# Kernel optimization log

Measured on AMD Instinct MI355X. Metric: run time of the kernel, lower is better.

## Reference

```python
import jax, jax.numpy as jnp
import numpy as np

N_NODES = 100000
N_EDGES = 1600000
IN_FEATS = 128
HIDDEN = 128


def _graph_conv(x, W, b, src, dst, n_nodes):
    # DGL GraphConv with norm='both': out = D_in^{-1/2} * A^T * (D_out^{-1/2} * x) @ W + b
    ones = jnp.ones((src.shape[0],), dtype=x.dtype)
    deg_out = jax.ops.segment_sum(ones, src, num_segments=n_nodes)
    deg_in = jax.ops.segment_sum(ones, dst, num_segments=n_nodes)
    norm_src = jax.lax.rsqrt(jnp.clip(deg_out, 1.0))  # [N]
    norm_dst = jax.lax.rsqrt(jnp.clip(deg_in, 1.0))   # [N]
    h = x @ W                                          # [N, F_out]
    msg = h[src] * norm_src[src][:, None]              # gather by edge src: [E, F_out]
    agg = jax.ops.segment_sum(msg, dst, num_segments=n_nodes)  # scatter-add to dst
    return agg * norm_dst[:, None] + b


def setup_inputs() -> dict:
    key = jax.random.key(0)
    ks = jax.random.split(key, 9)
    x = jax.random.normal(ks[0], (N_NODES, IN_FEATS), dtype=jnp.float32)
    src = jax.random.randint(ks[1], (N_EDGES,), 0, N_NODES, dtype=jnp.int32)
    dst = jax.random.randint(ks[2], (N_EDGES,), 0, N_NODES, dtype=jnp.int32)
    s1 = 1.0 / np.sqrt(IN_FEATS)
    s2 = 1.0 / np.sqrt(HIDDEN)
    W1 = jax.random.uniform(ks[3], (IN_FEATS, HIDDEN), jnp.float32, -s1, s1)
    b1 = jnp.zeros((HIDDEN,), jnp.float32)
    W2 = jax.random.uniform(ks[4], (HIDDEN, HIDDEN), jnp.float32, -s2, s2)
    b2 = jnp.zeros((HIDDEN,), jnp.float32)
    sp = 1.0 / np.sqrt(2 * HIDDEN)
    Wp = jax.random.uniform(ks[5], (2 * HIDDEN, 1), jnp.float32, -sp, sp)
    bp = jax.random.uniform(ks[6], (1,), jnp.float32, -sp, sp)
    return {"x": x, "W1": W1, "b1": b1, "W2": W2, "b2": b2,
            "Wp": Wp, "bp": bp, "src": src, "dst": dst}


def reference(x, W1, b1, W2, b2, Wp, bp, src, dst):
    n_nodes = x.shape[0]
    h = _graph_conv(x, W1, b1, src, dst, n_nodes)
    h = jax.nn.relu(h)
    h = _graph_conv(h, W2, b2, src, dst, n_nodes)  # final node embeddings [N, H]
    # predict_links on the same edge list: cat(h[u], h[v]) -> linear -> sigmoid
    edge_h = jnp.concatenate([h[src], h[dst]], axis=1)  # [E, 2H]
    scores = jax.nn.sigmoid(edge_h @ Wp + bp)           # [E, 1]
    return scores
```

## Files before the change

kernel.cpp:

```cpp
#include <hip/hip_runtime.h>
#include <cstdint>
#include <cstddef>

#define NN 100000
#define NE 1600000
#define F  128
#define NPAD 100352
#define NBUCK 3125
#define BCAPG 768
#define CHUNK 4167

typedef __attribute__((ext_vector_type(8))) short bf16x8;
typedef __attribute__((ext_vector_type(4))) float f32x4;

__device__ __forceinline__ unsigned short f2bf(float f) {
    unsigned u = __float_as_uint(f);
    unsigned r = (u + 0x7fffu + ((u >> 16) & 1u)) >> 16;
    return (unsigned short)r;
}
__device__ __forceinline__ void acc_bf8s(const uint4 v, const float ns, float* acc) {
    acc[0] += __uint_as_float(v.x << 16) * ns;
    acc[1] += __uint_as_float(v.x & 0xffff0000u) * ns;
    acc[2] += __uint_as_float(v.y << 16) * ns;
    acc[3] += __uint_as_float(v.y & 0xffff0000u) * ns;
    acc[4] += __uint_as_float(v.z << 16) * ns;
    acc[5] += __uint_as_float(v.z & 0xffff0000u) * ns;
    acc[6] += __uint_as_float(v.w << 16) * ns;
    acc[7] += __uint_as_float(v.w & 0xffff0000u) * ns;
}

__global__ void setup_kernel(int* __restrict__ gCur,
                             const float* __restrict__ W2, const float* __restrict__ Wp,
                             const float* __restrict__ b2, const float* __restrict__ bp,
                             float* __restrict__ consts, float2* __restrict__ V) {
    const int g = blockIdx.x;
    const int tid = threadIdx.x;
    if (g < 13) {
        const int b = g * 256 + tid;
        if (b < NBUCK) gCur[b] = b * BCAPG;
        return;
    }
    if (tid < 128) {
        float sa = 0.f, sc = 0.f;
        #pragma unroll 8
        for (int j = 0; j < F; ++j) {
            const float w = W2[tid * F + j];
            sa += w * Wp[j];
            sc += w * Wp[F + j];
        }
        V[tid] = make_float2(sa, sc);
    } else if (tid < 192) {
        const int l = tid - 128;
        const float2 bb = *(const float2*)&b2[2 * l];
        const float2 wa = *(const float2*)&Wp[2 * l];
        const float2 wc = *(const float2*)&Wp[F + 2 * l];
        float s = bb.x * (wa.x + wc.x) + bb.y * (wa.y + wc.y);
        #pragma unroll
        for (int m = 32; m > 0; m >>= 1) s += __shfl_xor(s, m);
        if (l == 0) consts[0] = s + bp[0];
    }
}

__global__ __launch_bounds__(256, 3)
void gemm1_fill_kernel(const float* __restrict__ in, const float* __restrict__ W,
                       unsigned short* __restrict__ out_bf,
                       const int* __restrict__ src, const int* __restrict__ dst,
                       int* __restrict__ deg_out, int* __restrict__ gCur,
                       int* __restrict__ srcPart) {
    __shared__ __align__(16) char smem[50016];

    const int g = blockIdx.x;
    const int tid = threadIdx.x;

    if (g & 1) {
        int* packedL = (int*)smem;
        unsigned short* bktL = (unsigned short*)(packedL + CHUNK);
        int* hist = (int*)(smem + 25008);
        int* curL = hist + NBUCK;
        const int e0 = (g >> 1) * CHUNK;
        const int nCh = min(CHUNK, NE - e0);
        for (int i = tid; i < NBUCK; i += 256) hist[i] = 0;
        __syncthreads();
        for (int i = tid; i < nCh; i += 256) {
            const int s = src[e0 + i];
            const int d = dst[e0 + i];
            atomicAdd(&deg_out[s], 1);
            const int bkt = d >> 5;
            atomicAdd(&hist[bkt], 1);
            packedL[i] = s | ((d & 31) << 17);
            bktL[i] = (unsigned short)bkt;
        }
        __syncthreads();
        for (int b = tid; b < NBUCK; b += 256) {
            const int c = hist[b];
            curL[b] = (c > 0) ? atomicAdd(&gCur[b], c) : 0;
        }
        __syncthreads();
        for (int i = tid; i < nCh; i += 256) {
            const int bkt = bktL[i];
            const int p = atomicAdd(&curL[bkt], 1);
            if (p < (bkt + 1) * BCAPG)
                srcPart[p] = packedL[i];
        }
        return;
    }

    char* A_s = smem;

    const int gid  = g >> 1;
    const int w    = tid >> 6;
    const int lane = tid & 63;
    const int ml   = lane & 15;
    const int quad = lane >> 4;

    bf16x8 Bf[4][2];
    #pragma unroll
    for (int kb = 0; kb < 4; ++kb) {
        #pragma unroll
        for (int nb = 0; nb < 2; ++nb) {
            const int n = 32 * w + nb * 16 + ml;
            const int k0 = kb * 32 + quad * 8;
            #pragma unroll
            for (int j = 0; j < 8; ++j)
                Bf[kb][nb][j] = (short)f2bf(W[(k0 + j) * F + n]);
        }
    }

    const int nTiles = NN / 32;
    for (int tile = gid; tile < nTiles; tile += 384) {
        const int row0 = tile * 32;
        __syncthreads();
        #pragma unroll
        for (int c = 0; c < 2; ++c) {
            const int i2 = tid + 256 * c;
            const int m  = i2 >> 4;
            const int o  = i2 & 15;
            const float* xr = &in[(size_t)(row0 + m) * F + o * 8];
            const float4 v0 = *(const float4*)xr;
            const float4 v1 = *(const float4*)(xr + 4);
            short h8[8];
            h8[0] = (short)f2bf(v0.x); h8[1] = (short)f2bf(v0.y);
            h8[2] = (short)f2bf(v0.z); h8[3] = (short)f2bf(v0.w);
            h8[4] = (short)f2bf(v1.x); h8[5] = (short)f2bf(v1.y);
            h8[6] = (short)f2bf(v1.z); h8[7] = (short)f2bf(v1.w);
            const int kb2 = o >> 2, q2 = o & 3, ml2 = m & 15, mh2 = m >> 4;
            const int fo = (((mh2 * 4 + kb2) * 64) + q2 * 16 + ml2) * 16;
            *(bf16x8*)(A_s + fo) = *(bf16x8*)h8;
        }
        __syncthreads();

        f32x4 acc00 = {0,0,0,0}, acc01 = {0,0,0,0}, acc10 = {0,0,0,0}, acc11 = {0,0,0,0};
        #pragma unroll
        for (int kb = 0; kb < 4; ++kb) {
            const bf16x8 ah0 = *(const bf16x8*)(A_s + (kb * 64 + lane) * 16);
            const bf16x8 ah1 = *(const bf16x8*)(A_s + ((4 + kb) * 64 + lane) * 16);
            acc00 = __builtin_amdgcn_mfma_f32_16x16x32_bf16(ah0, Bf[kb][0], acc00, 0, 0, 0);
            acc01 = __builtin_amdgcn_mfma_f32_16x16x32_bf16(ah0, Bf[kb][1], acc01, 0, 0, 0);
            acc10 = __builtin_amdgcn_mfma_f32_16x16x32_bf16(ah1, Bf[kb][0], acc10, 0, 0, 0);
            acc11 = __builtin_amdgcn_mfma_f32_16x16x32_bf16(ah1, Bf[kb][1], acc11, 0, 0, 0);
        }

        #pragma unroll
        for (int mh = 0; mh < 2; ++mh) {
            #pragma unroll
            for (int nb = 0; nb < 2; ++nb) {
                const f32x4 a = (mh == 0) ? (nb == 0 ? acc00 : acc01)
                                          : (nb == 0 ? acc10 : acc11);
                const int row = row0 + mh * 16 + quad * 4;
                const int col = 32 * w + nb * 16 + ml;
                #pragma unroll
                for (int r = 0; r < 4; ++r)
                    out_bf[(size_t)(row + r) * F + col] = f2bf(a[r]);
            }
        }
    }
}

__global__ void normsrc_kernel(const int* __restrict__ deg_out, float* __restrict__ norm_src, int nN) {
    const int n = blockIdx.x * blockDim.x + threadIdx.x;
    if (n < nN) norm_src[n] = rsqrtf((float)max(deg_out[n], 1));
}

__global__ __launch_bounds__(256)
void gather_sort_kernel(const unsigned short* __restrict__ hs,
                        int* __restrict__ srcPart, const int* __restrict__ gCur,
                        const float* __restrict__ norm_src, const float* __restrict__ bias,
                        const float2* __restrict__ V, float2* __restrict__ uw,
                        int* __restrict__ offs, int* __restrict__ ends,
                        float* __restrict__ norm_dst) {
    __shared__ int cnt[32];
    __shared__ int loc[32];
    __shared__ int cur[32];
    __shared__ int sortedL[BCAPG];

    const int b   = blockIdx.x;
    const int tid = threadIdx.x;
    const int nlo = b * 32;
    const int nCnt = min(32, NN - nlo);
    const int eBase = b * BCAPG;
    const int total = min(gCur[b] - eBase, BCAPG);

    if (tid < 32) cnt[tid] = 0;
    __syncthreads();
    for (int i = tid; i < total; i += 256)
        atomicAdd(&cnt[(srcPart[eBase + i] >> 17) & 31], 1);
    __syncthreads();
    if (tid < 32) loc[tid] = cnt[tid];
    __syncthreads();
    for (int off = 1; off < 32; off <<= 1) {
        int v = 0;
        if (tid < 32 && tid >= off) v = loc[tid - off];
        __syncthreads();
        if (tid < 32) loc[tid] += v;
        __syncthreads();
    }
    if (tid < 32) cur[tid] = loc[tid] - cnt[tid];
    if (tid < nCnt) {
        const int st = eBase + loc[tid] - cnt[tid];
        offs[nlo + tid] = st;
        ends[nlo + tid] = st + cnt[tid];
        norm_dst[nlo + tid] = rsqrtf((float)max(cnt[tid], 1));
    }
    __syncthreads();
    for (int i = tid; i < total; i += 256) {
        const int v = srcPart[eBase + i];
        const int r = atomicAdd(&cur[(v >> 17) & 31], 1);
        sortedL[r] = v & 0x1FFFF;
    }
    __syncthreads();
    for (int i = tid; i < total; i += 256)
        srcPart[eBase + i] = sortedL[i];

    const int w  = tid >> 6;
    const int l  = tid & 63;
    const int q  = l >> 4;
    const int c8 = (l & 15) * 8;
    float bb[8];
    *(float4*)&bb[0] = *(const float4*)&bias[c8];
    *(float4*)&bb[4] = *(const float4*)&bias[c8 + 4];
    float2 Vl[8];
    #pragma unroll
    for (int k = 0; k < 8; ++k) Vl[k] = V[c8 + k];

    const int nhEnd = min((w + 1) * 8, nCnt);
    for (int nh = w * 8; nh < nhEnd; ++nh) {
        const int end = loc[nh];
        const int beg = end - cnt[nh];
        float acc[8] = {0.f, 0.f, 0.f, 0.f, 0.f, 0.f, 0.f, 0.f};
        int j = beg;
        for (; j + 16 <= end; j += 16) {
            const int s0 = sortedL[j + q];
            const int s1 = sortedL[j + 4 + q];
            const int s2 = sortedL[j + 8 + q];
            const int s3 = sortedL[j + 12 + q];
            const float ns0 = norm_src[s0];
            const float ns1 = norm_src[s1];
            const float ns2 = norm_src[s2];
            const float ns3 = norm_src[s3];
            const uint4 v0 = *(const uint4*)&hs[(size_t)s0 * F + c8];
            const uint4 v1 = *(const uint4*)&hs[(size_t)s1 * F + c8];
            const uint4 v2 = *(const uint4*)&hs[(size_t)s2 * F + c8];
            const uint4 v3 = *(const uint4*)&hs[(size_t)s3 * F + c8];
            acc_bf8s(v0, ns0, acc);
            acc_bf8s(v1, ns1, acc);
            acc_bf8s(v2, ns2, acc);
            acc_bf8s(v3, ns3, acc);
        }
        for (; j + 8 <= end; j += 8) {
            const int s0 = sortedL[j + q];
            const int s1 = sortedL[j + 4 + q];
            const float ns0 = norm_src[s0];
            const float ns1 = norm_src[s1];
            const uint4 v0 = *(const uint4*)&hs[(size_t)s0 * F + c8];
            const uint4 v1 = *(const uint4*)&hs[(size_t)s1 * F + c8];
            acc_bf8s(v0, ns0, acc);
            acc_bf8s(v1, ns1, acc);
        }
        for (; j + 4 <= end; j += 4) {
            const int s = sortedL[j + q];
            const float ns = norm_src[s];
            const uint4 v = *(const uint4*)&hs[(size_t)s * F + c8];
            acc_bf8s(v, ns, acc);
        }
        if (j + q < end) {
            const int s = sortedL[j + q];
            const float ns = norm_src[s];
            const uint4 v = *(const uint4*)&hs[(size_t)s * F + c8];
            acc_bf8s(v, ns, acc);
        }
        #pragma unroll
        for (int k = 0; k < 8; ++k) {
            acc[k] += __shfl_xor(acc[k], 16);
            acc[k] += __shfl_xor(acc[k], 32);
        }

        const int n = nlo + nh;
        const float nd = rsqrtf((float)max(cnt[nh], 1));
        float pa = 0.f, pc = 0.f;
        #pragma unroll
        for (int k = 0; k < 8; ++k) {
            const float ok = fmaxf(acc[k] * nd + bb[k], 0.f);
            pa += ok * Vl[k].x;
            pc += ok * Vl[k].y;
        }
        #pragma unroll
        for (int m = 1; m <= 8; m <<= 1) {
            pa += __shfl_xor(pa, m);
            pc += __shfl_xor(pc, m);
        }
        if (l == 0) {
            const float ns = norm_src[n];
            uw[n] = make_float2(ns * pa, ns * pc);
        }
    }
}

__global__ void ac_kernel(const float2* __restrict__ uw, const int* __restrict__ sorted_src,
                          const int* __restrict__ offs, const int* __restrict__ ends,
                          const float* __restrict__ norm_dst,
                          float* __restrict__ A, float* __restrict__ C, int nN) {
    const int n = blockIdx.x * blockDim.x + threadIdx.x;
    if (n >= nN) return;
    const int beg = offs[n];
    const int end = ends[n];
    float su = 0.f, sw = 0.f;
    int j = beg;
    for (; j + 2 <= end; j += 2) {
        const float2 t0 = uw[sorted_src[j]];
        const float2 t1 = uw[sorted_src[j + 1]];
        su += t0.x + t1.x;
        sw += t0.y + t1.y;
    }
    if (j < end) {
        const float2 t = uw[sorted_src[j]];
        su += t.x;
        sw += t.y;
    }
    const float nd = norm_dst[n];
    A[n] = nd * su;
    C[n] = nd * sw;
}

__global__ void score_kernel(const float* __restrict__ A, const float* __restrict__ C,
                             const int4* __restrict__ src4, const int4* __restrict__ dst4,
                             const float* __restrict__ consts, float4* __restrict__ out4,
                             int nE4) {
    const int i = blockIdx.x * blockDim.x + threadIdx.x;
    if (i < nE4) {
        const int4 s = src4[i];
        const int4 d = dst4[i];
        const float cc = consts[0];
        float4 o;
        o.x = 1.f / (1.f + __expf(-(A[s.x] + C[d.x] + cc)));
        o.y = 1.f / (1.f + __expf(-(A[s.y] + C[d.y] + cc)));
        o.z = 1.f / (1.f + __expf(-(A[s.z] + C[d.z] + cc)));
        o.w = 1.f / (1.f + __expf(-(A[s.w] + C[d.w] + cc)));
        out4[i] = o;
    }
}

extern "C" void kernel_launch(void* const* d_in, const int* in_sizes, int n_in,
                              void* d_out, int out_size, void* d_ws, size_t ws_size,
                              hipStream_t stream) {
    const float* x  = (const float*)d_in[0];
    const float* W1 = (const float*)d_in[1];
    const float* b1 = (const float*)d_in[2];
    const float* W2 = (const float*)d_in[3];
    const float* b2 = (const float*)d_in[4];
    const float* Wp = (const float*)d_in[5];
    const float* bp = (const float*)d_in[6];
    const int*   src = (const int*)d_in[7];
    const int*   dst = (const int*)d_in[8];
    float* out = (float*)d_out;

    float* ws        = (float*)d_ws;
    float* norm_src  = ws;
    float* bufA      = ws + NPAD;
    float* bufC      = ws + 2 * NPAD;
    float* norm_dst  = ws + 3 * NPAD;
    int*   offs      = (int*)(ws + 4 * NPAD);
    int*   ends      = offs + NPAD;
    int*   gCur      = ends + NPAD;
    float* consts    = (float*)(gCur + 4096);
    float2* V        = (float2*)(consts + 16);
    float2* uw       = V + 128;
    int*   srcPart   = (int*)(uw + NN);
    unsigned short* hs_bf = (unsigned short*)(srcPart + (size_t)NBUCK * BCAPG);

    hipMemsetAsync(bufA, 0, NPAD * sizeof(int), stream);
    setup_kernel<<<14, 256, 0, stream>>>(gCur, W2, Wp, b2, bp, consts, V);

    gemm1_fill_kernel<<<768, 256, 0, stream>>>(x, W1, hs_bf, src, dst,
                                               (int*)bufA, gCur, srcPart);

    normsrc_kernel<<<(NN + 255) / 256, 256, 0, stream>>>((const int*)bufA, norm_src, NN);

    gather_sort_kernel<<<NBUCK, 256, 0, stream>>>(hs_bf, srcPart, gCur, norm_src, b1,
                                                  V, uw, offs, ends, norm_dst);

    ac_kernel<<<(NN + 255) / 256, 256, 0, stream>>>(uw, srcPart, offs, ends, norm_dst,
                                                    bufA, bufC, NN);

    score_kernel<<<(NE / 4 + 255) / 256, 256, 0, stream>>>(bufA, bufC, (const int4*)src,
                                                           (const int4*)dst, consts,
                                                           (float4*)out, NE / 4);
}
```

Measured before the change: 311.0 us.

## Fuse edge bucketing into every GEMM block and pad global bucket counters

Instead of splitting blocks between edge bucketing and GEMM work, every one of the 1536 blocks now bucket-fills a smaller edge chunk and then runs GEMM tiles. The per-chunk LDS staging of packed edges is dropped; src/dst are re-read from global memory in the second pass, which halves shared memory and lets occupancy rise to 6 blocks per CU. Global bucket cursors are strided by 16 ints to spread atomic contention across cache lines. The cost is more per-block histogram setup and more global atomics, since each block scans all 3125 buckets for a much smaller chunk.

```diff
diff --git a/kernel.cpp b/kernel.cpp
--- a/kernel.cpp
+++ b/kernel.cpp
@@ -8,7 +8,9 @@
 #define NPAD 100352
 #define NBUCK 3125
 #define BCAPG 768
-#define CHUNK 4167
+#define NBLK 1536
+#define CHUNK 1042
+#define GSTRIDE 16
 
 typedef __attribute__((ext_vector_type(8))) short bf16x8;
 typedef __attribute__((ext_vector_type(4))) float f32x4;
@@ -37,7 +39,7 @@
     const int tid = threadIdx.x;
     if (g < 13) {
         const int b = g * 256 + tid;
-        if (b < NBUCK) gCur[b] = b * BCAPG;
+        if (b < NBUCK) gCur[b * GSTRIDE] = b * BCAPG;
         return;
     }
     if (tid < 128) {
@@ -61,23 +63,21 @@
     }
 }
 
-__global__ __launch_bounds__(256, 3)
+__global__ __launch_bounds__(256, 6)
 void gemm1_fill_kernel(const float* __restrict__ in, const float* __restrict__ W,
                        unsigned short* __restrict__ out_bf,
                        const int* __restrict__ src, const int* __restrict__ dst,
                        int* __restrict__ deg_out, int* __restrict__ gCur,
                        int* __restrict__ srcPart) {
-    __shared__ __align__(16) char smem[50016];
+    __shared__ __align__(16) char smem[25008];
 
     const int g = blockIdx.x;
     const int tid = threadIdx.x;
 
-    if (g & 1) {
-        int* packedL = (int*)smem;
-        unsigned short* bktL = (unsigned short*)(packedL + CHUNK);
-        int* hist = (int*)(smem + 25008);
+    {
+        int* hist = (int*)smem;
         int* curL = hist + NBUCK;
-        const int e0 = (g >> 1) * CHUNK;
+        const int e0 = g * CHUNK;
         const int nCh = min(CHUNK, NE - e0);
         for (int i = tid; i < NBUCK; i += 256) hist[i] = 0;
         __syncthreads();
@@ -85,29 +85,26 @@
             const int s = src[e0 + i];
             const int d = dst[e0 + i];
             atomicAdd(&deg_out[s], 1);
-            const int bkt = d >> 5;
-            atomicAdd(&hist[bkt], 1);
-            packedL[i] = s | ((d & 31) << 17);
-            bktL[i] = (unsigned short)bkt;
+            atomicAdd(&hist[d >> 5], 1);
         }
         __syncthreads();
         for (int b = tid; b < NBUCK; b += 256) {
             const int c = hist[b];
-            curL[b] = (c > 0) ? atomicAdd(&gCur[b], c) : 0;
+            curL[b] = (c > 0) ? atomicAdd(&gCur[b * GSTRIDE], c) : 0;
         }
         __syncthreads();
         for (int i = tid; i < nCh; i += 256) {
-            const int bkt = bktL[i];
+            const int s = src[e0 + i];
+            const int d = dst[e0 + i];
+            const int bkt = d >> 5;
             const int p = atomicAdd(&curL[bkt], 1);
             if (p < (bkt + 1) * BCAPG)
-                srcPart[p] = packedL[i];
-        }
-        return;
+                srcPart[p] = s | ((d & 31) << 17);
+        }
     }
 
     char* A_s = smem;
 
-    const int gid  = g >> 1;
     const int w    = tid >> 6;
     const int lane = tid & 63;
     const int ml   = lane & 15;
@@ -127,7 +124,7 @@
     }
 
     const int nTiles = NN / 32;
-    for (int tile = gid; tile < nTiles; tile += 384) {
+    for (int tile = g; tile < nTiles; tile += NBLK) {
         const int row0 = tile * 32;
         __syncthreads();
         #pragma unroll
@@ -198,7 +195,7 @@
     const int nlo = b * 32;
     const int nCnt = min(32, NN - nlo);
     const int eBase = b * BCAPG;
-    const int total = min(gCur[b] - eBase, BCAPG);
+    const int total = min(gCur[b * GSTRIDE] - eBase, BCAPG);
 
     if (tid < 32) cnt[tid] = 0;
     __syncthreads();
@@ -381,7 +378,7 @@
     int*   offs      = (int*)(ws + 4 * NPAD);
     int*   ends      = offs + NPAD;
     int*   gCur      = ends + NPAD;
-    float* consts    = (float*)(gCur + 4096);
+    float* consts    = (float*)(gCur + 50176);
     float2* V        = (float2*)(consts + 16);
     float2* uw       = V + 128;
     int*   srcPart   = (int*)(uw + NN);
@@ -390,8 +387,8 @@
     hipMemsetAsync(bufA, 0, NPAD * sizeof(int), stream);
     setup_kernel<<<14, 256, 0, stream>>>(gCur, W2, Wp, b2, bp, consts, V);
 
-    gemm1_fill_kernel<<<768, 256, 0, stream>>>(x, W1, hs_bf, src, dst,
-                                               (int*)bufA, gCur, srcPart);
+    gemm1_fill_kernel<<<NBLK, 256, 0, stream>>>(x, W1, hs_bf, src, dst,
+                                                (int*)bufA, gCur, srcPart);
 
     normsrc_kernel<<<(NN + 255) / 256, 256, 0, stream>>>((const int*)bufA, norm_src, NN);
 
```

New measurement: 416.3 us. +33.9%, slower.

## Replace single-pass bucket scatter with two-level radix partition of edges

Applied to the files above, without the earlier changes.

The edge bucketing by destination is split into two passes. The first pass, fused with the GEMM, partitions edges into 49 coarse regions using a small shared histogram and writes contiguous runs. A new pass2 kernel then sub-partitions each region into 64 fine buckets. Global bucket counters are padded to a 16-int stride to cut atomic contention. This trades one extra kernel launch and an extra read/write of the edge array for fewer scattered global writes and a much smaller LDS histogram, which allows higher occupancy in the fill blocks.

```diff
diff --git a/kernel.cpp b/kernel.cpp
--- a/kernel.cpp
+++ b/kernel.cpp
@@ -9,6 +9,11 @@
 #define NBUCK 3125
 #define BCAPG 768
 #define CHUNK 4167
+#define GSTRIDE 16
+#define NREG 49
+#define RCAP 36864
+#define P2SPLIT 16
+#define P2MAX 2304
 
 typedef __attribute__((ext_vector_type(8))) short bf16x8;
 typedef __attribute__((ext_vector_type(4))) float f32x4;
@@ -29,7 +34,7 @@
     acc[7] += __uint_as_float(v.w & 0xffff0000u) * ns;
 }
 
-__global__ void setup_kernel(int* __restrict__ gCur,
+__global__ void setup_kernel(int* __restrict__ gCur, int* __restrict__ gRegCur,
                              const float* __restrict__ W2, const float* __restrict__ Wp,
                              const float* __restrict__ b2, const float* __restrict__ bp,
                              float* __restrict__ consts, float2* __restrict__ V) {
@@ -37,7 +42,7 @@
     const int tid = threadIdx.x;
     if (g < 13) {
         const int b = g * 256 + tid;
-        if (b < NBUCK) gCur[b] = b * BCAPG;
+        if (b < NBUCK) gCur[b * GSTRIDE] = b * BCAPG;
         return;
     }
     if (tid < 128) {
@@ -58,6 +63,9 @@
         #pragma unroll
         for (int m = 32; m > 0; m >>= 1) s += __shfl_xor(s, m);
         if (l == 0) consts[0] = s + bp[0];
+    } else if (tid < 192 + NREG) {
+        const int r = tid - 192;
+        gRegCur[r * GSTRIDE] = r * RCAP;
     }
 }
 
@@ -65,42 +73,53 @@
 void gemm1_fill_kernel(const float* __restrict__ in, const float* __restrict__ W,
                        unsigned short* __restrict__ out_bf,
                        const int* __restrict__ src, const int* __restrict__ dst,
-                       int* __restrict__ deg_out, int* __restrict__ gCur,
-                       int* __restrict__ srcPart) {
-    __shared__ __align__(16) char smem[50016];
+                       int* __restrict__ deg_out, int* __restrict__ gRegCur,
+                       int* __restrict__ gRegion) {
+    __shared__ __align__(16) char smem[21504];
 
     const int g = blockIdx.x;
     const int tid = threadIdx.x;
 
     if (g & 1) {
-        int* packedL = (int*)smem;
-        unsigned short* bktL = (unsigned short*)(packedL + CHUNK);
-        int* hist = (int*)(smem + 25008);
-        int* curL = hist + NBUCK;
+        int* sortedL = (int*)smem;
+        unsigned char* regOf = (unsigned char*)(sortedL + CHUNK);
+        int* cnt  = (int*)(smem + 20840);
+        int* cur  = cnt + NREG;
+        int* base = cur + NREG;
+
         const int e0 = (g >> 1) * CHUNK;
         const int nCh = min(CHUNK, NE - e0);
-        for (int i = tid; i < NBUCK; i += 256) hist[i] = 0;
+        if (tid < NREG) cnt[tid] = 0;
         __syncthreads();
         for (int i = tid; i < nCh; i += 256) {
             const int s = src[e0 + i];
             const int d = dst[e0 + i];
             atomicAdd(&deg_out[s], 1);
-            const int bkt = d >> 5;
-            atomicAdd(&hist[bkt], 1);
-            packedL[i] = s | ((d & 31) << 17);
-            bktL[i] = (unsigned short)bkt;
-        }
-        __syncthreads();
-        for (int b = tid; b < NBUCK; b += 256) {
-            const int c = hist[b];
-            curL[b] = (c > 0) ? atomicAdd(&gCur[b], c) : 0;
+            atomicAdd(&cnt[d >> 11], 1);
+        }
+        __syncthreads();
+        if (tid < NREG && cnt[tid] > 0)
+            base[tid] = atomicAdd(&gRegCur[tid * GSTRIDE], cnt[tid]);
+        if (tid == 0) {
+            int run = 0;
+            for (int r = 0; r < NREG; ++r) { cur[r] = run; run += cnt[r]; }
         }
         __syncthreads();
         for (int i = tid; i < nCh; i += 256) {
-            const int bkt = bktL[i];
-            const int p = atomicAdd(&curL[bkt], 1);
-            if (p < (bkt + 1) * BCAPG)
-                srcPart[p] = packedL[i];
+            const int s = src[e0 + i];
+            const int d = dst[e0 + i];
+            const int r = d >> 11;
+            const int p = atomicAdd(&cur[r], 1);
+            sortedL[p] = s | ((d & 0x7FF) << 17);
+            regOf[p] = (unsigned char)r;
+        }
+        __syncthreads();
+        for (int i = tid; i < nCh; i += 256) {
+            const int r = regOf[i];
+            const int start = cur[r] - cnt[r];
+            const int dstAbs = base[r] + (i - start);
+            if (dstAbs < (r + 1) * RCAP)
+                gRegion[dstAbs] = sortedL[i];
         }
         return;
     }
@@ -176,6 +195,64 @@
     }
 }
 
+__global__ __launch_bounds__(256)
+void pass2_kernel(const int* __restrict__ gRegion, const int* __restrict__ gRegCur,
+                  int* __restrict__ gCur, int* __restrict__ srcPart) {
+    __shared__ int sortedL[P2MAX];
+    __shared__ unsigned char fbOf[P2MAX];
+    __shared__ int cnt[64], cur[64], base[64];
+
+    const int r   = blockIdx.x / P2SPLIT;
+    const int j   = blockIdx.x % P2SPLIT;
+    const int tid = threadIdx.x;
+
+    const int total = min(gRegCur[r * GSTRIDE] - r * RCAP, RCAP);
+    const int per = (total + P2SPLIT - 1) / P2SPLIT;
+    const int i0 = j * per;
+    const int i1 = min(total, i0 + per);
+    const int n = i1 - i0;
+
+    if (tid < 64) cnt[tid] = 0;
+    __syncthreads();
+
+    int v[9];
+    #pragma unroll
+    for (int k = 0; k < 9; ++k) {
+        const int i = tid + k * 256;
+        if (i < n) {
+            const int vv = gRegion[r * RCAP + i0 + i];
+            v[k] = vv;
+            atomicAdd(&cnt[vv >> 22], 1);
+        }
+    }
+    __syncthreads();
+    if (tid < 64 && cnt[tid] > 0)
+        base[tid] = atomicAdd(&gCur[(r * 64 + tid) * GSTRIDE], cnt[tid]);
+    if (tid == 0) {
+        int run = 0;
+        for (int f = 0; f < 64; ++f) { cur[f] = run; run += cnt[f]; }
+    }
+    __syncthreads();
+    #pragma unroll
+    for (int k = 0; k < 9; ++k) {
+        const int i = tid + k * 256;
+        if (i < n) {
+            const int fb = v[k] >> 22;
+            const int p = atomicAdd(&cur[fb], 1);
+            sortedL[p] = v[k] & 0x3FFFFF;
+            fbOf[p] = (unsigned char)fb;
+        }
+    }
+    __syncthreads();
+    for (int i = tid; i < n; i += 256) {
+        const int fb = fbOf[i];
+        const int start = cur[fb] - cnt[fb];
+        const int dstAbs = base[fb] + (i - start);
+        if (dstAbs < (r * 64 + fb + 1) * BCAPG)
+            srcPart[dstAbs] = sortedL[i];
+    }
+}
+
 __global__ void normsrc_kernel(const int* __restrict__ deg_out, float* __restrict__ norm_src, int nN) {
     const int n = blockIdx.x * blockDim.x + threadIdx.x;
     if (n < nN) norm_src[n] = rsqrtf((float)max(deg_out[n], 1));
@@ -198,7 +275,7 @@
     const int nlo = b * 32;
     const int nCnt = min(32, NN - nlo);
     const int eBase = b * BCAPG;
-    const int total = min(gCur[b] - eBase, BCAPG);
+    const int total = min(gCur[b * GSTRIDE] - eBase, BCAPG);
 
     if (tid < 32) cnt[tid] = 0;
     __syncthreads();
@@ -381,17 +458,21 @@
     int*   offs      = (int*)(ws + 4 * NPAD);
     int*   ends      = offs + NPAD;
     int*   gCur      = ends + NPAD;
-    float* consts    = (float*)(gCur + 4096);
+    int*   gRegCur   = gCur + 50176;
+    float* consts    = (float*)(gRegCur + 1024);
     float2* V        = (float2*)(consts + 16);
     float2* uw       = V + 128;
     int*   srcPart   = (int*)(uw + NN);
     unsigned short* hs_bf = (unsigned short*)(srcPart + (size_t)NBUCK * BCAPG);
+    int*   gRegion   = (int*)(hs_bf + (size_t)NN * F);
 
     hipMemsetAsync(bufA, 0, NPAD * sizeof(int), stream);
-    setup_kernel<<<14, 256, 0, stream>>>(gCur, W2, Wp, b2, bp, consts, V);
+    setup_kernel<<<14, 256, 0, stream>>>(gCur, gRegCur, W2, Wp, b2, bp, consts, V);
 
     gemm1_fill_kernel<<<768, 256, 0, stream>>>(x, W1, hs_bf, src, dst,
-                                               (int*)bufA, gCur, srcPart);
+                                               (int*)bufA, gRegCur, gRegion);
+
+    pass2_kernel<<<NREG * P2SPLIT, 256, 0, stream>>>(gRegion, gRegCur, gCur, srcPart);
 
     normsrc_kernel<<<(NN + 255) / 256, 256, 0, stream>>>((const int*)bufA, norm_src, NN);
 
```

After: 306.6 us. Within noise of the previous version (-1.4%).
